# Kernel optimization log

Hardware: AMD Instinct MI355X
Metric: run time of the kernel (lower is better)

The kernel has to match this reference:

```python
import jax, jax.numpy as jnp
import numpy as np

N_S = 50000
N_T = 50000
E = 800000
D_IN = 128
D_OUT = 128


def setup_inputs() -> dict:
    key = jax.random.key(0)
    k1, k2, k3, k4 = jax.random.split(key, 4)
    edge_index = jax.random.randint(k1, (2, E), 0, N_S, dtype=jnp.int64)
    x_s = jax.random.normal(k2, (N_S, D_IN), dtype=jnp.float32)
    x_t = jax.random.normal(k3, (N_T, D_IN), dtype=jnp.float32)
    # glorot-ish linear weight of GCNConv (bias=False)
    W = jax.random.normal(k4, (D_IN, D_OUT), dtype=jnp.float32) * (1.0 / np.sqrt(D_IN))
    return {"edge_index": edge_index, "x_s": x_s, "x_t": x_t, "W": W}


def reference(edge_index, x_s, x_t, W):
    N_s = x_s.shape[0]
    N_t = x_t.shape[0]
    N = N_s + N_t
    # dropout p=0.0 -> identity; concat bipartite features
    x = jnp.concatenate([x_s, x_t], axis=0)  # [N, d_in]
    row = edge_index[0]
    col = edge_index[1] + N_s  # module shifts target indices in-place
    # GCNConv: add self-loops with weight 1
    loops = jnp.arange(N, dtype=row.dtype)
    row_f = jnp.concatenate([row, loops])
    col_f = jnp.concatenate([col, loops])
    w = jnp.ones(row_f.shape[0], dtype=x.dtype)
    # symmetric degree normalization: deg computed on target (col)
    deg = jax.ops.segment_sum(w, col_f, num_segments=N)
    deg_inv_sqrt = jnp.where(deg > 0, jax.lax.rsqrt(deg), 0.0)
    norm = deg_inv_sqrt[row_f] * deg_inv_sqrt[col_f]  # [E+N]
    # linear transform then normalized scatter-add aggregation
    h = x @ W  # [N, d_out]
    msg = h[row_f] * norm[:, None]  # gather + scale, [E+N, d_out]
    out = jax.ops.segment_sum(msg, col_f, num_segments=N)  # scatter-add
    out = jax.nn.relu(out)
    return out[:N_s], out[N_s:]
```

## Files before the change

### kernel.cpp

```cpp
#include <hip/hip_runtime.h>
#include <hip/hip_bf16.h>
#include <math.h>

#define NSRC 50000
#define NTGT 50000
#define NTOT 100000
#define NEDGE 800000
#define DIM 128
#define WPAD 136
#define GEMM_GRID 1563

#define NBUCK 196
#define PBLK 98
#define EPB 8192
#define EPT 8
#define BCAP 6144

typedef __attribute__((ext_vector_type(8))) short short8;
typedef __attribute__((ext_vector_type(4))) float float4v;

union U8 { short8 s; uint4 u; };

__device__ __forceinline__ unsigned short f2bf(float f) {
    unsigned u = __float_as_uint(f);
    unsigned r = (u + 0x7FFFu + ((u >> 16) & 1u)) >> 16;
    return (unsigned short)r;
}
__device__ __forceinline__ float bf2f(unsigned us) {
    return __uint_as_float(us << 16);
}
__device__ __forceinline__ unsigned pkbf(float lo, float hi) {
    __hip_bfloat162 b = __float22bfloat162_rn(make_float2(lo, hi));
    return *(unsigned*)&b;
}

__global__ void k_prep(const float* __restrict__ W, unsigned short* __restrict__ Wt,
                       int* __restrict__ bcnt) {
    int i = blockIdx.x * blockDim.x + threadIdx.x;
    if (i < NBUCK) bcnt[i] = 0;
    if (i < DIM * DIM) {
        int k = i >> 7, n = i & 127;
        Wt[n * DIM + k] = f2bf(W[i]);
    }
}

__global__ __launch_bounds__(1024) void k_part2(const int* __restrict__ row,
                                                const int* __restrict__ col,
                                                int* __restrict__ bcnt,
                                                unsigned* __restrict__ part) {
    __shared__ int hist[NBUCK], runbase[NBUCK], cur[NBUCK];
    int tid = threadIdx.x;
    if (tid < NBUCK) hist[tid] = 0;
    __syncthreads();

    int e0 = blockIdx.x * EPB + tid * EPT;
    bool valid = (e0 + EPT <= NEDGE);
    int c[EPT], r[EPT];
    if (valid) {
        *(int4*)&c[0] = *(const int4*)(col + e0);
        *(int4*)&c[4] = *(const int4*)(col + e0 + 4);
        *(int4*)&r[0] = *(const int4*)(row + e0);
        *(int4*)&r[4] = *(const int4*)(row + e0 + 4);
#pragma unroll
        for (int i = 0; i < EPT; ++i) atomicAdd(&hist[c[i] >> 8], 1);
    }
    __syncthreads();
    if (tid < NBUCK) {
        runbase[tid] = atomicAdd(&bcnt[tid], hist[tid]);
        cur[tid] = 0;
    }
    __syncthreads();
    if (valid) {
#pragma unroll
        for (int i = 0; i < EPT; ++i) {
            int q = c[i] >> 8;
            int pos = runbase[q] + atomicAdd(&cur[q], 1);
            part[q * BCAP + pos] = (unsigned)r[i] | ((unsigned)(c[i] & 255) << 16);
        }
    }
}

__global__ __launch_bounds__(1024) void k_bucket(const int* __restrict__ bcnt,
                                                 const unsigned* __restrict__ part,
                                                 unsigned short* __restrict__ csr,
                                                 int* __restrict__ tstart,
                                                 int* __restrict__ tcnt) {
    __shared__ unsigned ebuf[BCAP];
    __shared__ unsigned short srt[BCAP];
    __shared__ int hist[256], bufA[256], bufB[256], cur[256];

    int q = blockIdx.x, tid = threadIdx.x;
    int n = bcnt[q];
    int base = q * BCAP;

    if (tid < 256) hist[tid] = 0;
    __syncthreads();
    for (int i = tid; i < n; i += 1024) {
        unsigned p = part[base + i];
        ebuf[i] = p;
        atomicAdd(&hist[p >> 16], 1);
    }
    __syncthreads();

    if (tid < 256) bufA[tid] = hist[tid];
    int* src = bufA; int* dst = bufB;
    for (int d = 1; d < 256; d <<= 1) {
        __syncthreads();
        if (tid < 256) dst[tid] = src[tid] + ((tid >= d) ? src[tid - d] : 0);
        int* t = src; src = dst; dst = t;
    }
    __syncthreads();
    if (tid < 256) {
        int excl = src[tid] - hist[tid];
        cur[tid] = excl;
        int c = q * 256 + tid;
        if (c < NTGT) {
            tstart[c] = base + excl;
            tcnt[c] = hist[tid];
        }
    }
    __syncthreads();

    for (int i = tid; i < n; i += 1024) {
        unsigned p = ebuf[i];
        int pos = atomicAdd(&cur[p >> 16], 1);
        srt[pos] = (unsigned short)(p & 0xffffu);
    }
    __syncthreads();
    int m = (n + 1) >> 1;
    unsigned* dst32 = (unsigned*)(csr + base);
    for (int i = tid; i < m; i += 1024) dst32[i] = ((unsigned*)srt)[i];
}

__global__ __launch_bounds__(256) void k_gemm(const float* __restrict__ xsrc,
                                              const float* __restrict__ xtgt,
                                              const unsigned short* __restrict__ Wt,
                                              unsigned short* __restrict__ h,
                                              float* __restrict__ out) {
    __shared__ unsigned short Bs[128 * WPAD];

    const int tid = threadIdx.x;
    for (int idx = tid; idx < 2048; idx += 256) {
        int n = idx >> 4, c8 = idx & 15;
        *(uint4*)&Bs[n * WPAD + c8 * 8] = *(const uint4*)(Wt + n * DIM + c8 * 8);
    }

    const int wave = tid >> 6, lane = tid & 63;
    const int nl = lane & 15, quad = lane >> 4;

    int node = blockIdx.x * 64 + wave * 16 + nl;
    int mc = (node < NTOT) ? node : (NTOT - 1);
    const float* xrow = (mc < NSRC) ? (xsrc + (size_t)mc * DIM)
                                    : (xtgt + (size_t)(mc - NSRC) * DIM);
    float4 a[8];
#pragma unroll
    for (int s = 0; s < 4; ++s) {
        a[2 * s]     = *(const float4*)(xrow + s * 32 + quad * 8);
        a[2 * s + 1] = *(const float4*)(xrow + s * 32 + quad * 8 + 4);
    }
    __syncthreads();

    float4v acc[8];
#pragma unroll
    for (int t = 0; t < 8; ++t) acc[t] = (float4v){0.f, 0.f, 0.f, 0.f};

#pragma unroll
    for (int s = 0; s < 4; ++s) {
        U8 af;
        af.u.x = pkbf(a[2 * s].x, a[2 * s].y);
        af.u.y = pkbf(a[2 * s].z, a[2 * s].w);
        af.u.z = pkbf(a[2 * s + 1].x, a[2 * s + 1].y);
        af.u.w = pkbf(a[2 * s + 1].z, a[2 * s + 1].w);
#pragma unroll
        for (int t = 0; t < 8; ++t) {
            short8 bf = *(const short8*)&Bs[(t * 16 + nl) * WPAD + s * 32 + quad * 8];
            acc[t] = __builtin_amdgcn_mfma_f32_16x16x32_bf16(bf, af.s, acc[t], 0, 0, 0);
        }
    }

    if (node < NTOT) {
        unsigned short* hp = h + (size_t)node * DIM + quad * 4;
        float* op = out + (size_t)node * DIM + quad * 4;
        bool isrc = (node < NSRC);
#pragma unroll
        for (int t = 0; t < 8; ++t) {
            uint2 p;
            p.x = pkbf(acc[t][0], acc[t][1]);
            p.y = pkbf(acc[t][2], acc[t][3]);
            *(uint2*)(hp + t * 16) = p;
            if (isrc) {
                float4 o;
                o.x = fmaxf(acc[t][0], 0.f);
                o.y = fmaxf(acc[t][1], 0.f);
                o.z = fmaxf(acc[t][2], 0.f);
                o.w = fmaxf(acc[t][3], 0.f);
                *(float4*)(op + t * 16) = o;
            }
        }
    }
}

__global__ __launch_bounds__(256) void k_agg(const int* __restrict__ tstart,
                                             const int* __restrict__ tcnt,
                                             const unsigned short* __restrict__ csr,
                                             const unsigned short* __restrict__ h,
                                             float* __restrict__ out) {
    int w = threadIdx.x >> 6;
    int lane = threadIdx.x & 63;
    int c = blockIdx.x * 4 + w;
    if (c >= NTGT) return;

    int n = tcnt[c];
    int s0 = tstart[c];
    int q = lane >> 4;
    int ql = lane & 15;

    float acc[8];
#pragma unroll
    for (int i = 0; i < 8; ++i) acc[i] = 0.f;

    int j = 0;
    while (j < n) {
        int nb = (n - j < 64) ? (n - j) : 64;
        int v = (lane < nb) ? (int)csr[s0 + j + lane] : 0;
        int n4 = nb & ~3;
        int kk = 0;
#pragma unroll 4
        for (; kk < n4; kk += 4) {
            int r = __shfl(v, kk + q, 64);
            uint4 d = *(const uint4*)(h + (size_t)r * DIM + ql * 8);
            acc[0] += bf2f(d.x & 0xffff); acc[1] += bf2f(d.x >> 16);
            acc[2] += bf2f(d.y & 0xffff); acc[3] += bf2f(d.y >> 16);
            acc[4] += bf2f(d.z & 0xffff); acc[5] += bf2f(d.z >> 16);
            acc[6] += bf2f(d.w & 0xffff); acc[7] += bf2f(d.w >> 16);
        }
        int rem = nb - kk;
        if (rem) {
            int qq = (q < rem) ? q : 0;
            int r = __shfl(v, kk + qq, 64);
            if (q < rem) {
                uint4 d = *(const uint4*)(h + (size_t)r * DIM + ql * 8);
                acc[0] += bf2f(d.x & 0xffff); acc[1] += bf2f(d.x >> 16);
                acc[2] += bf2f(d.y & 0xffff); acc[3] += bf2f(d.y >> 16);
                acc[4] += bf2f(d.z & 0xffff); acc[5] += bf2f(d.z >> 16);
                acc[6] += bf2f(d.w & 0xffff); acc[7] += bf2f(d.w >> 16);
            }
        }
        j += nb;
    }

#pragma unroll
    for (int i = 0; i < 8; ++i) {
        acc[i] += __shfl_xor(acc[i], 16, 64);
        acc[i] += __shfl_xor(acc[i], 32, 64);
    }

    if (q == 0) {
        float di = rsqrtf(1.0f + (float)n);
        float dd = di * di;
        uint4 dh = *(const uint4*)(h + (size_t)(NSRC + c) * DIM + ql * 8);
        float4 o0, o1;
        o0.x = fmaxf(di * acc[0] + dd * bf2f(dh.x & 0xffff), 0.f);
        o0.y = fmaxf(di * acc[1] + dd * bf2f(dh.x >> 16), 0.f);
        o0.z = fmaxf(di * acc[2] + dd * bf2f(dh.y & 0xffff), 0.f);
        o0.w = fmaxf(di * acc[3] + dd * bf2f(dh.y >> 16), 0.f);
        o1.x = fmaxf(di * acc[4] + dd * bf2f(dh.z & 0xffff), 0.f);
        o1.y = fmaxf(di * acc[5] + dd * bf2f(dh.z >> 16), 0.f);
        o1.z = fmaxf(di * acc[6] + dd * bf2f(dh.w & 0xffff), 0.f);
        o1.w = fmaxf(di * acc[7] + dd * bf2f(dh.w >> 16), 0.f);
        float* op = out + (size_t)(NSRC + c) * DIM + ql * 8;
        *(float4*)op = o0;
        *(float4*)(op + 4) = o1;
    }
}

extern "C" void kernel_launch(void* const* d_in, const int* in_sizes, int n_in,
                              void* d_out, int out_size, void* d_ws, size_t ws_size,
                              hipStream_t stream) {
    const int* ei     = (const int*)d_in[0];
    const float* xsrc = (const float*)d_in[1];
    const float* xtgt = (const float*)d_in[2];
    const float* W    = (const float*)d_in[3];
    float* out = (float*)d_out;

    const int* row = ei;
    const int* col = ei + NEDGE;

    char* ws = (char*)d_ws;
    unsigned short* h  = (unsigned short*)ws;  ws += (size_t)NTOT * DIM * 2;
    unsigned short* Wt = (unsigned short*)ws;  ws += DIM * DIM * 2;
    unsigned* part = (unsigned*)ws;            ws += (size_t)NBUCK * BCAP * 4;
    unsigned short* csr = (unsigned short*)ws; ws += (size_t)NBUCK * BCAP * 2;
    int* bcnt   = (int*)ws;                    ws += NBUCK * 4;
    int* tstart = (int*)ws;                    ws += NTGT * 4;
    int* tcnt   = (int*)ws;                    ws += NTGT * 4;

    k_prep<<<(DIM * DIM + 255) / 256, 256, 0, stream>>>(W, Wt, bcnt);
    k_part2<<<PBLK, 1024, 0, stream>>>(row, col, bcnt, part);
    k_bucket<<<NBUCK, 1024, 0, stream>>>(bcnt, part, csr, tstart, tcnt);
    k_gemm<<<GEMM_GRID, 256, 0, stream>>>(xsrc, xtgt, Wt, h, out);
    k_agg<<<(NTGT + 3) / 4, 256, 0, stream>>>(tstart, tcnt, csr, h, out);
}
```

Before: 165.6 us.

## Fuse edge partitioning and GEMM into one heterogeneous front kernel

Merges the edge bucket-partition pass and the dense x@W GEMM into a single launch. The first blocks partition edges and the remaining blocks do the GEMM, so the two independent stages run concurrently. The separate W transpose/convert kernel is dropped: each GEMM block converts W to bf16 into shared memory itself, and the bucket counters are cleared with a memset. This removes launches and lets the latency-bound partition overlap with the GEMM, at the cost of every GEMM block redundantly reading and converting W, and smaller partition blocks doing more global atomics.

After: 185.7 us. +12.1%, slower.

```diff
diff --git a/kernel.cpp b/kernel.cpp
--- a/kernel.cpp
+++ b/kernel.cpp
@@ -8,24 +8,20 @@
 #define NEDGE 800000
 #define DIM 128
 #define WPAD 136
+
+#define NBUCK 196
+#define BCAP 6144
+#define EPT 8
+#define EPB2 2048
+#define PBLK2 391
 #define GEMM_GRID 1563
-
-#define NBUCK 196
-#define PBLK 98
-#define EPB 8192
-#define EPT 8
-#define BCAP 6144
+#define FGRID (PBLK2 + GEMM_GRID)
 
 typedef __attribute__((ext_vector_type(8))) short short8;
 typedef __attribute__((ext_vector_type(4))) float float4v;
 
 union U8 { short8 s; uint4 u; };
 
-__device__ __forceinline__ unsigned short f2bf(float f) {
-    unsigned u = __float_as_uint(f);
-    unsigned r = (u + 0x7FFFu + ((u >> 16) & 1u)) >> 16;
-    return (unsigned short)r;
-}
 __device__ __forceinline__ float bf2f(unsigned us) {
     return __uint_as_float(us << 16);
 }
@@ -34,121 +30,77 @@
     return *(unsigned*)&b;
 }
 
-__global__ void k_prep(const float* __restrict__ W, unsigned short* __restrict__ Wt,
-                       int* __restrict__ bcnt) {
-    int i = blockIdx.x * blockDim.x + threadIdx.x;
-    if (i < NBUCK) bcnt[i] = 0;
-    if (i < DIM * DIM) {
-        int k = i >> 7, n = i & 127;
-        Wt[n * DIM + k] = f2bf(W[i]);
-    }
-}
-
-__global__ __launch_bounds__(1024) void k_part2(const int* __restrict__ row,
-                                                const int* __restrict__ col,
-                                                int* __restrict__ bcnt,
-                                                unsigned* __restrict__ part) {
-    __shared__ int hist[NBUCK], runbase[NBUCK], cur[NBUCK];
-    int tid = threadIdx.x;
-    if (tid < NBUCK) hist[tid] = 0;
-    __syncthreads();
-
-    int e0 = blockIdx.x * EPB + tid * EPT;
-    bool valid = (e0 + EPT <= NEDGE);
-    int c[EPT], r[EPT];
-    if (valid) {
-        *(int4*)&c[0] = *(const int4*)(col + e0);
-        *(int4*)&c[4] = *(const int4*)(col + e0 + 4);
-        *(int4*)&r[0] = *(const int4*)(row + e0);
-        *(int4*)&r[4] = *(const int4*)(row + e0 + 4);
-#pragma unroll
-        for (int i = 0; i < EPT; ++i) atomicAdd(&hist[c[i] >> 8], 1);
-    }
-    __syncthreads();
-    if (tid < NBUCK) {
-        runbase[tid] = atomicAdd(&bcnt[tid], hist[tid]);
-        cur[tid] = 0;
-    }
-    __syncthreads();
-    if (valid) {
-#pragma unroll
-        for (int i = 0; i < EPT; ++i) {
-            int q = c[i] >> 8;
-            int pos = runbase[q] + atomicAdd(&cur[q], 1);
-            part[q * BCAP + pos] = (unsigned)r[i] | ((unsigned)(c[i] & 255) << 16);
-        }
-    }
-}
-
-__global__ __launch_bounds__(1024) void k_bucket(const int* __restrict__ bcnt,
-                                                 const unsigned* __restrict__ part,
-                                                 unsigned short* __restrict__ csr,
-                                                 int* __restrict__ tstart,
-                                                 int* __restrict__ tcnt) {
-    __shared__ unsigned ebuf[BCAP];
-    __shared__ unsigned short srt[BCAP];
-    __shared__ int hist[256], bufA[256], bufB[256], cur[256];
-
-    int q = blockIdx.x, tid = threadIdx.x;
-    int n = bcnt[q];
-    int base = q * BCAP;
-
-    if (tid < 256) hist[tid] = 0;
-    __syncthreads();
-    for (int i = tid; i < n; i += 1024) {
-        unsigned p = part[base + i];
-        ebuf[i] = p;
-        atomicAdd(&hist[p >> 16], 1);
-    }
-    __syncthreads();
-
-    if (tid < 256) bufA[tid] = hist[tid];
-    int* src = bufA; int* dst = bufB;
-    for (int d = 1; d < 256; d <<= 1) {
+__global__ __launch_bounds__(256) void k_front(const int* __restrict__ row,
+                                               const int* __restrict__ col,
+                                               int* __restrict__ bcnt,
+                                               unsigned* __restrict__ part,
+                                               const float* __restrict__ xsrc,
+                                               const float* __restrict__ xtgt,
+                                               const float* __restrict__ W,
+                                               unsigned short* __restrict__ h,
+                                               float* __restrict__ out) {
+    __shared__ union SM {
+        struct { int hist[NBUCK]; int runbase[NBUCK]; int cur[NBUCK]; } p;
+        unsigned short Bs[128 * WPAD];
+    } sm;
+
+    const int tid = threadIdx.x;
+
+    if (blockIdx.x < PBLK2) {
+        if (tid < NBUCK) sm.p.hist[tid] = 0;
         __syncthreads();
-        if (tid < 256) dst[tid] = src[tid] + ((tid >= d) ? src[tid - d] : 0);
-        int* t = src; src = dst; dst = t;
-    }
-    __syncthreads();
-    if (tid < 256) {
-        int excl = src[tid] - hist[tid];
-        cur[tid] = excl;
-        int c = q * 256 + tid;
-        if (c < NTGT) {
-            tstart[c] = base + excl;
-            tcnt[c] = hist[tid];
-        }
-    }
-    __syncthreads();
-
-    for (int i = tid; i < n; i += 1024) {
-        unsigned p = ebuf[i];
-        int pos = atomicAdd(&cur[p >> 16], 1);
-        srt[pos] = (unsigned short)(p & 0xffffu);
-    }
-    __syncthreads();
-    int m = (n + 1) >> 1;
-    unsigned* dst32 = (unsigned*)(csr + base);
-    for (int i = tid; i < m; i += 1024) dst32[i] = ((unsigned*)srt)[i];
-}
-
-__global__ __launch_bounds__(256) void k_gemm(const float* __restrict__ xsrc,
-                                              const float* __restrict__ xtgt,
-                                              const unsigned short* __restrict__ Wt,
-                                              unsigned short* __restrict__ h,
-                                              float* __restrict__ out) {
-    __shared__ unsigned short Bs[128 * WPAD];
-
-    const int tid = threadIdx.x;
-    for (int idx = tid; idx < 2048; idx += 256) {
-        int n = idx >> 4, c8 = idx & 15;
-        *(uint4*)&Bs[n * WPAD + c8 * 8] = *(const uint4*)(Wt + n * DIM + c8 * 8);
+
+        int e0 = blockIdx.x * EPB2 + tid * EPT;
+        bool valid = (e0 + EPT <= NEDGE);
+        int c[EPT], r[EPT];
+        if (valid) {
+            *(int4*)&c[0] = *(const int4*)(col + e0);
+            *(int4*)&c[4] = *(const int4*)(col + e0 + 4);
+            *(int4*)&r[0] = *(const int4*)(row + e0);
+            *(int4*)&r[4] = *(const int4*)(row + e0 + 4);
+#pragma unroll
+            for (int i = 0; i < EPT; ++i) atomicAdd(&sm.p.hist[c[i] >> 8], 1);
+        }
+        __syncthreads();
+        if (tid < NBUCK) {
+            sm.p.runbase[tid] = atomicAdd(&bcnt[tid], sm.p.hist[tid]);
+            sm.p.cur[tid] = 0;
+        }
+        __syncthreads();
+        if (valid) {
+#pragma unroll
+            for (int i = 0; i < EPT; ++i) {
+                int q = c[i] >> 8;
+                int pos = sm.p.runbase[q] + atomicAdd(&sm.p.cur[q], 1);
+                part[q * BCAP + pos] = (unsigned)r[i] | ((unsigned)(c[i] & 255) << 16);
+            }
+        }
+        return;
+    }
+
+    const int gb = blockIdx.x - PBLK2;
+
+#pragma unroll 2
+    for (int rr = 0; rr < 8; ++rr) {
+        int task = rr * 256 + tid;
+        int kp = task >> 5;
+        int g = task & 31;
+        const float* w0 = W + (2 * kp) * DIM + g * 4;
+        float4 f0 = *(const float4*)w0;
+        float4 f1 = *(const float4*)(w0 + DIM);
+        const float* f0p = (const float*)&f0;
+        const float* f1p = (const float*)&f1;
+#pragma unroll
+        for (int jj = 0; jj < 4; ++jj) {
+            int j = (jj + g) & 3;
+            *(unsigned*)&sm.Bs[(g * 4 + j) * WPAD + 2 * kp] = pkbf(f0p[j], f1p[j]);
+        }
     }
 
     const int wave = tid >> 6, lane = tid & 63;
     const int nl = lane & 15, quad = lane >> 4;
 
-    int node = blockIdx.x * 64 + wave * 16 + nl;
+    int node = gb * 64 + wave * 16 + nl;
     int mc = (node < NTOT) ? node : (NTOT - 1);
     const float* xrow = (mc < NSRC) ? (xsrc + (size_t)mc * DIM)
                                     : (xtgt + (size_t)(mc - NSRC) * DIM);
@@ -173,7 +125,7 @@
         af.u.w = pkbf(a[2 * s + 1].z, a[2 * s + 1].w);
 #pragma unroll
         for (int t = 0; t < 8; ++t) {
-            short8 bf = *(const short8*)&Bs[(t * 16 + nl) * WPAD + s * 32 + quad * 8];
+            short8 bf = *(const short8*)&sm.Bs[(t * 16 + nl) * WPAD + s * 32 + quad * 8];
             acc[t] = __builtin_amdgcn_mfma_f32_16x16x32_bf16(bf, af.s, acc[t], 0, 0, 0);
         }
     }
@@ -198,6 +150,58 @@
             }
         }
     }
+}
+
+__global__ __launch_bounds__(1024) void k_bucket(const int* __restrict__ bcnt,
+                                                 const unsigned* __restrict__ part,
+                                                 unsigned short* __restrict__ csr,
+                                                 int* __restrict__ tstart,
+                                                 int* __restrict__ tcnt) {
+    __shared__ unsigned ebuf[BCAP];
+    __shared__ unsigned short srt[BCAP];
+    __shared__ int hist[256], bufA[256], bufB[256], cur[256];
+
+    int q = blockIdx.x, tid = threadIdx.x;
+    int n = bcnt[q];
+    int base = q * BCAP;
+
+    if (tid < 256) hist[tid] = 0;
+    __syncthreads();
+    for (int i = tid; i < n; i += 1024) {
+        unsigned p = part[base + i];
+        ebuf[i] = p;
+        atomicAdd(&hist[p >> 16], 1);
+    }
+    __syncthreads();
+
+    if (tid < 256) bufA[tid] = hist[tid];
+    int* src = bufA; int* dst = bufB;
+    for (int d = 1; d < 256; d <<= 1) {
+        __syncthreads();
+        if (tid < 256) dst[tid] = src[tid] + ((tid >= d) ? src[tid - d] : 0);
+        int* t = src; src = dst; dst = t;
+    }
+    __syncthreads();
+    if (tid < 256) {
+        int excl = src[tid] - hist[tid];
+        cur[tid] = excl;
+        int c = q * 256 + tid;
+        if (c < NTGT) {
+            tstart[c] = base + excl;
+            tcnt[c] = hist[tid];
+        }
+    }
+    __syncthreads();
+
+    for (int i = tid; i < n; i += 1024) {
+        unsigned p = ebuf[i];
+        int pos = atomicAdd(&cur[p >> 16], 1);
+        srt[pos] = (unsigned short)(p & 0xffffu);
+    }
+    __syncthreads();
+    int m = (n + 1) >> 1;
+    unsigned* dst32 = (unsigned*)(csr + base);
+    for (int i = tid; i < m; i += 1024) dst32[i] = ((unsigned*)srt)[i];
 }
 
 __global__ __launch_bounds__(256) void k_agg(const int* __restrict__ tstart,
@@ -288,16 +292,14 @@
 
     char* ws = (char*)d_ws;
     unsigned short* h  = (unsigned short*)ws;  ws += (size_t)NTOT * DIM * 2;
-    unsigned short* Wt = (unsigned short*)ws;  ws += DIM * DIM * 2;
     unsigned* part = (unsigned*)ws;            ws += (size_t)NBUCK * BCAP * 4;
     unsigned short* csr = (unsigned short*)ws; ws += (size_t)NBUCK * BCAP * 2;
     int* bcnt   = (int*)ws;                    ws += NBUCK * 4;
     int* tstart = (int*)ws;                    ws += NTGT * 4;
     int* tcnt   = (int*)ws;                    ws += NTGT * 4;
 
-    k_prep<<<(DIM * DIM + 255) / 256, 256, 0, stream>>>(W, Wt, bcnt);
-    k_part2<<<PBLK, 1024, 0, stream>>>(row, col, bcnt, part);
+    hipMemsetAsync(bcnt, 0, NBUCK * sizeof(int), stream);
+    k_front<<<FGRID, 256, 0, stream>>>(row, col, bcnt, part, xsrc, xtgt, W, h, out);
     k_bucket<<<NBUCK, 1024, 0, stream>>>(bcnt, part, csr, tstart, tcnt);
-    k_gemm<<<GEMM_GRID, 256, 0, stream>>>(xsrc, xtgt, Wt, h, out);
     k_agg<<<(NTGT + 3) / 4, 256, 0, stream>>>(tstart, tcnt, csr, h, out);
 }
```

## Fuse edge partitioning with GEMM in one launch and use finer buckets

Applied to the files above, without the earlier changes.

Merges the edge-partition kernel and the dense bf16 GEMM into a single heterogeneous grid, where the first blocks partition edges and the rest do the transform. The two independent stages can then run concurrently, and one launch is removed. Buckets shrink from 256 to 64 targets, with 782 buckets and 256-thread blocks, so the bucket-sort stage has more, smaller blocks and better occupancy. The cost is more global atomics on bucket counters, and a shared-memory union sized for the GEMM tile that may limit occupancy in the partition blocks.

Result: slower. 172.5 us (+4.2%).

```diff
diff --git a/kernel.cpp b/kernel.cpp
--- a/kernel.cpp
+++ b/kernel.cpp
@@ -8,13 +8,14 @@
 #define NEDGE 800000
 #define DIM 128
 #define WPAD 136
+
+#define NBUCK 782
+#define BCAP 1536
+#define EPT 8
+#define EPB2 2048
+#define PBLK2 391
 #define GEMM_GRID 1563
-
-#define NBUCK 196
-#define PBLK 98
-#define EPB 8192
-#define EPT 8
-#define BCAP 6144
+#define FGRID (PBLK2 + GEMM_GRID)
 
 typedef __attribute__((ext_vector_type(8))) short short8;
 typedef __attribute__((ext_vector_type(4))) float float4v;
@@ -44,111 +45,65 @@
     }
 }
 
-__global__ __launch_bounds__(1024) void k_part2(const int* __restrict__ row,
-                                                const int* __restrict__ col,
-                                                int* __restrict__ bcnt,
-                                                unsigned* __restrict__ part) {
-    __shared__ int hist[NBUCK], runbase[NBUCK], cur[NBUCK];
-    int tid = threadIdx.x;
-    if (tid < NBUCK) hist[tid] = 0;
-    __syncthreads();
-
-    int e0 = blockIdx.x * EPB + tid * EPT;
-    bool valid = (e0 + EPT <= NEDGE);
-    int c[EPT], r[EPT];
-    if (valid) {
-        *(int4*)&c[0] = *(const int4*)(col + e0);
-        *(int4*)&c[4] = *(const int4*)(col + e0 + 4);
-        *(int4*)&r[0] = *(const int4*)(row + e0);
-        *(int4*)&r[4] = *(const int4*)(row + e0 + 4);
-#pragma unroll
-        for (int i = 0; i < EPT; ++i) atomicAdd(&hist[c[i] >> 8], 1);
-    }
-    __syncthreads();
-    if (tid < NBUCK) {
-        runbase[tid] = atomicAdd(&bcnt[tid], hist[tid]);
-        cur[tid] = 0;
-    }
-    __syncthreads();
-    if (valid) {
-#pragma unroll
-        for (int i = 0; i < EPT; ++i) {
-            int q = c[i] >> 8;
-            int pos = runbase[q] + atomicAdd(&cur[q], 1);
-            part[q * BCAP + pos] = (unsigned)r[i] | ((unsigned)(c[i] & 255) << 16);
-        }
-    }
-}
-
-__global__ __launch_bounds__(1024) void k_bucket(const int* __restrict__ bcnt,
-                                                 const unsigned* __restrict__ part,
-                                                 unsigned short* __restrict__ csr,
-                                                 int* __restrict__ tstart,
-                                                 int* __restrict__ tcnt) {
-    __shared__ unsigned ebuf[BCAP];
-    __shared__ unsigned short srt[BCAP];
-    __shared__ int hist[256], bufA[256], bufB[256], cur[256];
-
-    int q = blockIdx.x, tid = threadIdx.x;
-    int n = bcnt[q];
-    int base = q * BCAP;
-
-    if (tid < 256) hist[tid] = 0;
-    __syncthreads();
-    for (int i = tid; i < n; i += 1024) {
-        unsigned p = part[base + i];
-        ebuf[i] = p;
-        atomicAdd(&hist[p >> 16], 1);
-    }
-    __syncthreads();
-
-    if (tid < 256) bufA[tid] = hist[tid];
-    int* src = bufA; int* dst = bufB;
-    for (int d = 1; d < 256; d <<= 1) {
+__global__ __launch_bounds__(256) void k_front(const int* __restrict__ row,
+                                               const int* __restrict__ col,
+                                               int* __restrict__ bcnt,
+                                               unsigned* __restrict__ part,
+                                               const float* __restrict__ xsrc,
+                                               const float* __restrict__ xtgt,
+                                               const unsigned short* __restrict__ Wt,
+                                               unsigned short* __restrict__ h,
+                                               float* __restrict__ out) {
+    __shared__ union SM {
+        struct { int hist[NBUCK]; int runbase[NBUCK]; int cur[NBUCK]; } p;
+        unsigned short Bs[128 * WPAD];
+    } sm;
+
+    const int tid = threadIdx.x;
+
+    if (blockIdx.x < PBLK2) {
+        for (int i = tid; i < NBUCK; i += 256) sm.p.hist[i] = 0;
         __syncthreads();
-        if (tid < 256) dst[tid] = src[tid] + ((tid >= d) ? src[tid - d] : 0);
-        int* t = src; src = dst; dst = t;
-    }
-    __syncthreads();
-    if (tid < 256) {
-        int excl = src[tid] - hist[tid];
-        cur[tid] = excl;
-        int c = q * 256 + tid;
-        if (c < NTGT) {
-            tstart[c] = base + excl;
-            tcnt[c] = hist[tid];
-        }
-    }
-    __syncthreads();
-
-    for (int i = tid; i < n; i += 1024) {
-        unsigned p = ebuf[i];
-        int pos = atomicAdd(&cur[p >> 16], 1);
-        srt[pos] = (unsigned short)(p & 0xffffu);
-    }
-    __syncthreads();
-    int m = (n + 1) >> 1;
-    unsigned* dst32 = (unsigned*)(csr + base);
-    for (int i = tid; i < m; i += 1024) dst32[i] = ((unsigned*)srt)[i];
-}
-
-__global__ __launch_bounds__(256) void k_gemm(const float* __restrict__ xsrc,
-                                              const float* __restrict__ xtgt,
-                                              const unsigned short* __restrict__ Wt,
-                                              unsigned short* __restrict__ h,
-                                              float* __restrict__ out) {
-    __shared__ unsigned short Bs[128 * WPAD];
-
-    const int tid = threadIdx.x;
+
+        int e0 = blockIdx.x * EPB2 + tid * EPT;
+        bool valid = (e0 + EPT <= NEDGE);
+        int c[EPT], r[EPT];
+        if (valid) {
+            *(int4*)&c[0] = *(const int4*)(col + e0);
+            *(int4*)&c[4] = *(const int4*)(col + e0 + 4);
+            *(int4*)&r[0] = *(const int4*)(row + e0);
+            *(int4*)&r[4] = *(const int4*)(row + e0 + 4);
+#pragma unroll
+            for (int i = 0; i < EPT; ++i) atomicAdd(&sm.p.hist[c[i] >> 6], 1);
+        }
+        __syncthreads();
+        for (int i = tid; i < NBUCK; i += 256) {
+            sm.p.runbase[i] = atomicAdd(&bcnt[i], sm.p.hist[i]);
+            sm.p.cur[i] = 0;
+        }
+        __syncthreads();
+        if (valid) {
+#pragma unroll
+            for (int i = 0; i < EPT; ++i) {
+                int q = c[i] >> 6;
+                int pos = sm.p.runbase[q] + atomicAdd(&sm.p.cur[q], 1);
+                part[q * BCAP + pos] = (unsigned)r[i] | ((unsigned)(c[i] & 63) << 16);
+            }
+        }
+        return;
+    }
+
+    const int gb = blockIdx.x - PBLK2;
+
     for (int idx = tid; idx < 2048; idx += 256) {
         int n = idx >> 4, c8 = idx & 15;
-        *(uint4*)&Bs[n * WPAD + c8 * 8] = *(const uint4*)(Wt + n * DIM + c8 * 8);
+        *(uint4*)&sm.Bs[n * WPAD + c8 * 8] = *(const uint4*)(Wt + n * DIM + c8 * 8);
     }
 
     const int wave = tid >> 6, lane = tid & 63;
     const int nl = lane & 15, quad = lane >> 4;
 
-    int node = blockIdx.x * 64 + wave * 16 + nl;
+    int node = gb * 64 + wave * 16 + nl;
     int mc = (node < NTOT) ? node : (NTOT - 1);
     const float* xrow = (mc < NSRC) ? (xsrc + (size_t)mc * DIM)
                                     : (xtgt + (size_t)(mc - NSRC) * DIM);
@@ -173,7 +128,7 @@
         af.u.w = pkbf(a[2 * s + 1].z, a[2 * s + 1].w);
 #pragma unroll
         for (int t = 0; t < 8; ++t) {
-            short8 bf = *(const short8*)&Bs[(t * 16 + nl) * WPAD + s * 32 + quad * 8];
+            short8 bf = *(const short8*)&sm.Bs[(t * 16 + nl) * WPAD + s * 32 + quad * 8];
             acc[t] = __builtin_amdgcn_mfma_f32_16x16x32_bf16(bf, af.s, acc[t], 0, 0, 0);
         }
     }
@@ -198,6 +153,58 @@
             }
         }
     }
+}
+
+__global__ __launch_bounds__(256) void k_bucket(const int* __restrict__ bcnt,
+                                                const unsigned* __restrict__ part,
+                                                unsigned short* __restrict__ csr,
+                                                int* __restrict__ tstart,
+                                                int* __restrict__ tcnt) {
+    __shared__ unsigned ebuf[BCAP];
+    __shared__ unsigned short srt[BCAP];
+    __shared__ int hist[64], bufA[64], bufB[64], cur[64];
+
+    int q = blockIdx.x, tid = threadIdx.x;
+    int n = bcnt[q];
+    int base = q * BCAP;
+
+    if (tid < 64) hist[tid] = 0;
+    __syncthreads();
+    for (int i = tid; i < n; i += 256) {
+        unsigned p = part[base + i];
+        ebuf[i] = p;
+        atomicAdd(&hist[p >> 16], 1);
+    }
+    __syncthreads();
+
+    if (tid < 64) bufA[tid] = hist[tid];
+    int* src = bufA; int* dst = bufB;
+    for (int d = 1; d < 64; d <<= 1) {
+        __syncthreads();
+        if (tid < 64) dst[tid] = src[tid] + ((tid >= d) ? src[tid - d] : 0);
+        int* t = src; src = dst; dst = t;
+    }
+    __syncthreads();
+    if (tid < 64) {
+        int excl = src[tid] - hist[tid];
+        cur[tid] = excl;
+        int c = q * 64 + tid;
+        if (c < NTGT) {
+            tstart[c] = base + excl;
+            tcnt[c] = hist[tid];
+        }
+    }
+    __syncthreads();
+
+    for (int i = tid; i < n; i += 256) {
+        unsigned p = ebuf[i];
+        int pos = atomicAdd(&cur[p >> 16], 1);
+        srt[pos] = (unsigned short)(p & 0xffffu);
+    }
+    __syncthreads();
+    int m = (n + 1) >> 1;
+    unsigned* dst32 = (unsigned*)(csr + base);
+    for (int i = tid; i < m; i += 256) dst32[i] = ((unsigned*)srt)[i];
 }
 
 __global__ __launch_bounds__(256) void k_agg(const int* __restrict__ tstart,
@@ -296,8 +303,7 @@
     int* tcnt   = (int*)ws;                    ws += NTGT * 4;
 
     k_prep<<<(DIM * DIM + 255) / 256, 256, 0, stream>>>(W, Wt, bcnt);
-    k_part2<<<PBLK, 1024, 0, stream>>>(row, col, bcnt, part);
-    k_bucket<<<NBUCK, 1024, 0, stream>>>(bcnt, part, csr, tstart, tcnt);
-    k_gemm<<<GEMM_GRID, 256, 0, stream>>>(xsrc, xtgt, Wt, h, out);
+    k_front<<<FGRID, 256, 0, stream>>>(row, col, bcnt, part, xsrc, xtgt, Wt, h, out);
+    k_bucket<<<NBUCK, 256, 0, stream>>>(bcnt, part, csr, tstart, tcnt);
     k_agg<<<(NTGT + 3) / 4, 256, 0, stream>>>(tstart, tcnt, csr, h, out);
 }
```
